# Kernel tuning notes

Hardware: AMD Instinct MI355X
Metric: run time of the kernel (lower is better)

## Reference

```python
import jax, jax.numpy as jnp
import numpy as np

N_NODES = 10000
N_EDGES = 160000
N_GRAPHS = 64
D_IN = 128
D_H = 512
N_CLS = 2
L = 3
EPS = 1e-7   # GENConv message eps / clamp min
MAXV = 10.0  # GENConv power-mean clamp max
BN_EPS = 1e-5


def setup_inputs() -> dict:
    key = jax.random.key(0)
    ks = jax.random.split(key, 8)
    return {
        "x": jax.random.normal(ks[0], (N_NODES, D_IN), jnp.float32),
        "W0": jax.random.normal(ks[1], (D_IN, D_H), jnp.float32) * 0.05,
        "Wrest": jax.random.normal(ks[2], (L - 1, D_H, D_H), jnp.float32) * 0.05,
        "bconv": jnp.zeros((L, D_H), jnp.float32),
        "p": jnp.ones((L,), jnp.float32),
        "msg_scale": jnp.ones((L,), jnp.float32),
        "bn_gamma": jnp.ones((L, D_H), jnp.float32),
        "bn_beta": jnp.zeros((L, D_H), jnp.float32),
        "fc1_W": jax.random.normal(ks[3], (2 * D_H, D_H), jnp.float32) * 0.05,
        "fc1_b": jnp.zeros((D_H,), jnp.float32),
        "bn4_g": jnp.ones((D_H,), jnp.float32),
        "bn4_b": jnp.zeros((D_H,), jnp.float32),
        "fc2_W": jax.random.normal(ks[4], (D_H, N_CLS), jnp.float32) * 0.05,
        "fc2_b": jnp.zeros((N_CLS,), jnp.float32),
        "edge_index": jax.random.randint(ks[5], (2, N_EDGES), 0, N_NODES, dtype=jnp.int32),
        "batch": jnp.sort(jax.random.randint(ks[6], (N_NODES,), 0, N_GRAPHS, dtype=jnp.int32)),
    }


def _batchnorm(h, g, b):
    # training-mode BatchNorm1d: batch statistics, biased variance
    mu = h.mean(axis=0)
    var = ((h - mu) ** 2).mean(axis=0)
    return (h - mu) * jax.lax.rsqrt(var + BN_EPS) * g + b


def _genconv(x, W, b, p, scale, src, dst):
    # message: m_e = relu(x_src) + eps  (no edge_attr), clamped to [eps, 10]
    m = jnp.minimum(jax.nn.relu(x[src]) + EPS, MAXV)          # [E, d]
    # power-mean aggregation onto target nodes
    deg = jax.ops.segment_sum(jnp.ones((src.shape[0],), x.dtype), dst, N_NODES)
    agg = jax.ops.segment_sum(m ** p, dst, N_NODES) / jnp.maximum(deg, 1.0)[:, None]
    agg = jnp.clip(agg, EPS, MAXV) ** (1.0 / p)               # [N, d]
    # MessageNorm: l2-normalize aggregated message, rescale by ||x|| * scale
    msg = agg / jnp.maximum(jnp.linalg.norm(agg, axis=-1, keepdims=True), 1e-12)
    xn = jnp.linalg.norm(x, axis=-1, keepdims=True)
    out = x + msg * xn * scale                                # residual add
    return out @ W + b                                        # 1-layer MLP


def reference(x, W0, Wrest, bconv, p, msg_scale, bn_gamma, bn_beta,
              fc1_W, fc1_b, bn4_g, bn4_b, fc2_W, fc2_b, edge_index, batch):
    src, dst = edge_index[0], edge_index[1]
    h = x
    jk = None
    for i in range(L):
        W = W0 if i == 0 else Wrest[i - 1]
        h = _genconv(h, W, bconv[i], p[i], msg_scale[i], src, dst)
        h = jax.nn.relu(_batchnorm(h, bn_gamma[i], bn_beta[i]))
        jk = h if jk is None else jnp.maximum(jk, h)          # JumpingKnowledge 'max'
    # global max + mean pooling per graph
    cnt = jax.ops.segment_sum(jnp.ones((N_NODES,), h.dtype), batch, N_GRAPHS)
    gmean = jax.ops.segment_sum(jk, batch, N_GRAPHS) / jnp.maximum(cnt, 1.0)[:, None]
    gmax = jax.ops.segment_max(jk, batch, N_GRAPHS)
    gmax = jnp.where(cnt[:, None] > 0, gmax, 0.0)
    g = jnp.concatenate([gmax, gmean], axis=1)                # [G, 1024]
    g = jax.nn.relu(_batchnorm(g @ fc1_W + fc1_b, bn4_g, bn4_b))
    # dropout: eval mode (identity)
    return g @ fc2_W + fc2_b                                  # [G, num_classes]
```

## Files before the change

### kernel.cpp

```cpp
#include <hip/hip_runtime.h>
#include <hip/hip_bf16.h>
#include <math.h>

#define N_NODES 10000
#define N_GRAPHS 64
#define N_EDGES 160000
#define D_INPUT 128
#define D_H 512
#define EPS 1e-7f
#define MAXV 10.0f
#define BN_EPS 1e-5f
#define M_PAD 10112

typedef __attribute__((ext_vector_type(4))) float f32x4;
typedef __attribute__((ext_vector_type(8))) __bf16 bf16x8;

__global__ __launch_bounds__(256) void hist_kernel(const int* __restrict__ dst,
                                                   int* __restrict__ cnt) {
  int i = blockIdx.x * blockDim.x + threadIdx.x;
  if (i < N_EDGES) atomicAdd(&cnt[dst[i]], 1);
}

__global__ __launch_bounds__(256) void scan_kernel(int* __restrict__ cnt,
                                                   int* __restrict__ rowptr) {
  __shared__ int ps[256];
  int tid = threadIdx.x;
  const int CH = 40;
  int b0 = tid * CH;
  bool active = (b0 < N_NODES);
  int v[CH];
  int s = 0;
  if (active) {
    const int4* c4p = (const int4*)(cnt + b0);
#pragma unroll
    for (int i = 0; i < CH / 4; i++) {
      int4 q = c4p[i];
      v[4 * i] = q.x; v[4 * i + 1] = q.y; v[4 * i + 2] = q.z; v[4 * i + 3] = q.w;
      s += q.x + q.y + q.z + q.w;
    }
  }
  ps[tid] = s;
  __syncthreads();
  for (int off = 1; off < 256; off <<= 1) {
    int t = (tid >= off) ? ps[tid - off] : 0;
    __syncthreads();
    ps[tid] += t;
    __syncthreads();
  }
  int run = (tid == 0) ? 0 : ps[tid - 1];
  if (active) {
    int r[CH];
#pragma unroll
    for (int i = 0; i < CH; i++) { r[i] = run; run += v[i]; }
    int4* rp = (int4*)(rowptr + b0);
    int4* cz = (int4*)(cnt + b0);
#pragma unroll
    for (int i = 0; i < CH / 4; i++) {
      rp[i] = make_int4(r[4 * i], r[4 * i + 1], r[4 * i + 2], r[4 * i + 3]);
      cz[i] = make_int4(0, 0, 0, 0);
    }
  }
  if (tid == 255) rowptr[N_NODES] = ps[255];
}

__global__ __launch_bounds__(256) void scatter_kernel(
    const int* __restrict__ src, const int* __restrict__ dst,
    const int* __restrict__ rowptr, int* __restrict__ cursor,
    int* __restrict__ csr_src) {
  int i = blockIdx.x * blockDim.x + threadIdx.x;
  if (i < N_EDGES) {
    int t = dst[i];
    int pos = rowptr[t] + atomicAdd(&cursor[t], 1);
    csr_src[pos] = src[i];
  }
}

__global__ __launch_bounds__(512) void bn_affine(float* __restrict__ stats,
                                                 const float* __restrict__ gamma,
                                                 const float* __restrict__ beta,
                                                 float* __restrict__ aff) {
  int c = threadIdx.x;
  const float invN = 1.0f / (float)N_NODES;
  float mean = stats[c] * invN;
  float var = stats[D_H + c] * invN - mean * mean;
  float sc = rsqrtf(var + BN_EPS) * gamma[c];
  aff[c] = sc;
  aff[D_H + c] = beta[c] - mean * sc;
  stats[c] = 0.f;
  stats[D_H + c] = 0.f;
}

__global__ __launch_bounds__(256) void msg0_kernel(const float* __restrict__ x,
                                                   const float* __restrict__ p_ptr,
                                                   __hip_bfloat16* __restrict__ msgb) {
  float p = *p_ptr;
  bool p1 = (p == 1.0f);
  const int total = N_NODES * D_INPUT / 2;
  for (int i = blockIdx.x * 256 + threadIdx.x; i < total; i += gridDim.x * 256) {
    float2 v = ((const float2*)x)[i];
    float m0 = fminf(fmaxf(v.x, 0.f) + EPS, MAXV);
    float m1 = fminf(fmaxf(v.y, 0.f) + EPS, MAXV);
    if (!p1) { m0 = powf(m0, p); m1 = powf(m1, p); }
    __hip_bfloat162 o;
    o.x = __float2bfloat16(m0);
    o.y = __float2bfloat16(m1);
    ((__hip_bfloat162*)msgb)[i] = o;
  }
}

template <int D, bool BN>
__global__ __launch_bounds__(256) void agg_msgnorm_kernel(
    const float* __restrict__ h, const float* __restrict__ aff,
    const __hip_bfloat16* __restrict__ msgb,
    const int* __restrict__ rowptr, const int* __restrict__ csr_src,
    const float* __restrict__ p_ptr, const float* __restrict__ scale_ptr,
    __hip_bfloat16* __restrict__ out) {
  constexpr int C = D / 2;
  constexpr int SL = 256 / C;
  int n = blockIdx.x;
  int tid = threadIdx.x;
  int col = tid % C;
  int slice = tid / C;
  int lo = rowptr[n], hi = rowptr[n + 1];
  float p = *p_ptr;
  float scale = *scale_ptr;
  bool p1 = (p == 1.0f);
  float invp = 1.0f / p;
  float inv_dg = 1.0f / fmaxf((float)(hi - lo), 1.0f);
  const float2* h2 = (const float2*)h;
  const uint* mg = (const uint*)msgb;

  __shared__ int s_src[256];
  float accx = 0.f, accy = 0.f;
  for (int base = lo; base < hi; base += 256) {
    int m = min(256, hi - base);
    __syncthreads();
    if (tid < m) s_src[tid] = csr_src[base + tid];
    __syncthreads();
    int j = slice;
    for (; j + 3 * SL < m; j += 4 * SL) {
      uint u0 = mg[(size_t)s_src[j] * C + col];
      uint u1 = mg[(size_t)s_src[j + SL] * C + col];
      uint u2 = mg[(size_t)s_src[j + 2 * SL] * C + col];
      uint u3 = mg[(size_t)s_src[j + 3 * SL] * C + col];
      accx += (__uint_as_float(u0 << 16) + __uint_as_float(u1 << 16)) +
              (__uint_as_float(u2 << 16) + __uint_as_float(u3 << 16));
      accy += (__uint_as_float(u0 & 0xFFFF0000u) + __uint_as_float(u1 & 0xFFFF0000u)) +
              (__uint_as_float(u2 & 0xFFFF0000u) + __uint_as_float(u3 & 0xFFFF0000u));
    }
    for (; j < m; j += SL) {
      uint u = mg[(size_t)s_src[j] * C + col];
      accx += __uint_as_float(u << 16);
      accy += __uint_as_float(u & 0xFFFF0000u);
    }
  }

  if constexpr (SL > 1) {
    __shared__ float sacc[2][256];
    sacc[0][tid] = accx;
    sacc[1][tid] = accy;
    __syncthreads();
    if (tid < C) {
#pragma unroll
      for (int s = 1; s < SL; s++) {
        accx += sacc[0][s * C + tid];
        accy += sacc[1][s * C + tid];
      }
    }
  }

  float a0 = 0.f, a1 = 0.f, hv0 = 0.f, hv1 = 0.f, sa = 0.f, sh = 0.f;
  if (tid < C) {
    a0 = fminf(fmaxf(accx * inv_dg, EPS), MAXV);
    a1 = fminf(fmaxf(accy * inv_dg, EPS), MAXV);
    if (!p1) { a0 = powf(a0, invp); a1 = powf(a1, invp); }
    float2 hx = h2[(size_t)n * C + tid];
    if constexpr (BN) {
      float2 s2 = ((const float2*)aff)[tid];
      float2 b2 = ((const float2*)(aff + D_H))[tid];
      hx.x = fmaxf(hx.x * s2.x + b2.x, 0.f);
      hx.y = fmaxf(hx.y * s2.y + b2.y, 0.f);
    }
    hv0 = hx.x;
    hv1 = hx.y;
    sa = a0 * a0 + a1 * a1;
    sh = hv0 * hv0 + hv1 * hv1;
  }
  for (int off = 32; off; off >>= 1) {
    sa += __shfl_down(sa, off);
    sh += __shfl_down(sh, off);
  }
  __shared__ float red[2][4];
  __shared__ float tot[2];
  int wid = tid >> 6;
  if ((tid & 63) == 0) { red[0][wid] = sa; red[1][wid] = sh; }
  __syncthreads();
  if (tid == 0) {
    tot[0] = red[0][0] + red[0][1] + red[0][2] + red[0][3];
    tot[1] = red[1][0] + red[1][1] + red[1][2] + red[1][3];
  }
  __syncthreads();
  float k = sqrtf(tot[1]) * scale / fmaxf(sqrtf(tot[0]), 1e-12f);
  if (tid < C) {
    __hip_bfloat162 o2;
    o2.x = __float2bfloat16(hv0 + a0 * k);
    o2.y = __float2bfloat16(hv1 + a1 * k);
    ((__hip_bfloat162*)out)[(size_t)n * C + tid] = o2;
  }
}

__global__ __launch_bounds__(256) void convert_all(
    const float* __restrict__ W0, const float* __restrict__ Wrest,
    __hip_bfloat16* __restrict__ w0t, __hip_bfloat16* __restrict__ w1t,
    __hip_bfloat16* __restrict__ w2t, int* __restrict__ cnt,
    float* __restrict__ stats) {
  int z = blockIdx.z;
  const float* W;
  __hip_bfloat16* Wt;
  int K;
  if (z == 0) { W = W0; Wt = w0t; K = D_INPUT; }
  else if (z == 1) { W = Wrest; Wt = w1t; K = D_H; }
  else { W = Wrest + (size_t)D_H * D_H; Wt = w2t; K = D_H; }

  if (z == 0 && blockIdx.x >= 4) {
    int bid = (blockIdx.x - 4) * 16 + blockIdx.y;
    int idx = bid * 256 + threadIdx.x;
    if (idx < N_NODES) cnt[idx] = 0;
    int sidx = idx - N_NODES;
    if (sidx >= 0 && sidx < 1024) stats[sidx] = 0.f;
    return;
  }

  __shared__ float tile[32][33];
  int k0 = blockIdx.x * 32, n0 = blockIdx.y * 32;
  int tx = threadIdx.x & 31, ty = threadIdx.x >> 5;
  for (int i = ty; i < 32; i += 8)
    tile[i][tx] = W[(size_t)(k0 + i) * D_H + n0 + tx];
  __syncthreads();
  for (int i = ty; i < 32; i += 8)
    Wt[(size_t)(n0 + i) * K + k0 + tx] = __float2bfloat16(tile[tx][i]);
}

__global__ __launch_bounds__(256) void mfma_gemm(
    const __hip_bfloat16* __restrict__ A, const __hip_bfloat16* __restrict__ Bt,
    const float* __restrict__ bias, float* __restrict__ C, float* __restrict__ stats,
    int M, int K) {
  __shared__ ushort As[128 * 64];
  __shared__ ushort Bs[128 * 64];
  __shared__ float sred[128][2];
  int tid = threadIdx.x;
  int l = tid & 63;
  int w = tid >> 6;
  int wm = w >> 1, wn = w & 1;
  int row0 = blockIdx.x * 128;
  int col0 = blockIdx.y * 128;

  f32x4 acc[4][4];
#pragma unroll
  for (int m = 0; m < 4; m++)
#pragma unroll
    for (int n = 0; n < 4; n++) acc[m][n] = (f32x4){0.f, 0.f, 0.f, 0.f};

  const ushort* Ag = (const ushort*)A;
  const ushort* Bg = (const ushort*)Bt;
  char* AsB = (char*)As;
  char* BsB = (char*)Bs;

  if (tid < 128) { sred[tid][0] = 0.f; sred[tid][1] = 0.f; }

  int srow = tid >> 3;
  int scb = (tid & 7) * 16;
  int wbyte = scb ^ ((srow & 7) << 4);
  int scol = scb >> 1;

  int lswz = (l & 7) << 4;
  int kb = (l >> 4) * 16;
  int arow = wm * 64 + (l & 15);
  int brow = wn * 64 + (l & 15);

  for (int k0 = 0; k0 < K; k0 += 64) {
    uint4 ra[4], rb[4];
#pragma unroll
    for (int j = 0; j < 4; j++) {
      int row = j * 32 + srow;
      ra[j] = *(const uint4*)(Ag + (size_t)(row0 + row) * K + k0 + scol);
      rb[j] = *(const uint4*)(Bg + (size_t)(col0 + row) * K + k0 + scol);
    }
#pragma unroll
    for (int j = 0; j < 4; j++) {
      int row = j * 32 + srow;
      *(uint4*)(AsB + row * 128 + wbyte) = ra[j];
      *(uint4*)(BsB + row * 128 + wbyte) = rb[j];
    }
    __syncthreads();
#pragma unroll
    for (int kk = 0; kk < 2; kk++) {
      bf16x8 af[4], bfr[4];
#pragma unroll
      for (int m = 0; m < 4; m++)
        af[m] = *(const bf16x8*)(AsB + (arow + m * 16) * 128 + ((kk * 64 + kb) ^ lswz));
#pragma unroll
      for (int n = 0; n < 4; n++)
        bfr[n] = *(const bf16x8*)(BsB + (brow + n * 16) * 128 + ((kk * 64 + kb) ^ lswz));
#pragma unroll
      for (int m = 0; m < 4; m++)
#pragma unroll
        for (int n = 0; n < 4; n++)
          acc[m][n] = __builtin_amdgcn_mfma_f32_16x16x32_bf16(af[m], bfr[n], acc[m][n], 0, 0, 0);
    }
    __syncthreads();
  }

  int crow0 = row0 + wm * 64 + (l >> 4) * 4;
  int ccol0 = col0 + wn * 64 + (l & 15);
#pragma unroll
  for (int n = 0; n < 4; n++) {
    int col = ccol0 + n * 16;
    float bv = bias[col];
    float ps = 0.f, pq = 0.f;
#pragma unroll
    for (int m = 0; m < 4; m++) {
#pragma unroll
      for (int r = 0; r < 4; r++) {
        int rr = crow0 + m * 16 + r;
        if (rr < M) {
          float v = acc[m][n][r] + bv;
          C[(size_t)rr * D_H + col] = v;
          ps += v;
          pq += v * v;
        }
      }
    }
    ps += __shfl_down(ps, 16); pq += __shfl_down(pq, 16);
    ps += __shfl_down(ps, 32); pq += __shfl_down(pq, 32);
    if ((l >> 4) == 0) {
      atomicAdd(&sred[wn * 64 + n * 16 + (l & 15)][0], ps);
      atomicAdd(&sred[wn * 64 + n * 16 + (l & 15)][1], pq);
    }
  }
  __syncthreads();
  if (tid < 128) {
    atomicAdd(&stats[col0 + tid], sred[tid][0]);
    atomicAdd(&stats[D_H + col0 + tid], sred[tid][1]);
  }
}

template <bool WRITE_MSG>
__global__ __launch_bounds__(256) void jk_msg_update(
    const float* __restrict__ hlin, const float* __restrict__ aff,
    float* __restrict__ jk, const float* __restrict__ p_ptr,
    __hip_bfloat16* __restrict__ msgb, int layer) {
  float p = 1.f;
  bool p1 = true;
  if constexpr (WRITE_MSG) {
    p = *p_ptr;
    p1 = (p == 1.0f);
  }
  const int total = N_NODES * D_H / 4;
  for (int idx = blockIdx.x * blockDim.x + threadIdx.x; idx < total;
       idx += gridDim.x * blockDim.x) {
    int c4 = idx & 127;
    float4 x = ((const float4*)hlin)[idx];
    float4 sc = ((const float4*)aff)[c4];
    float4 sh = ((const float4*)(aff + D_H))[c4];
    float4 v;
    v.x = fmaxf(x.x * sc.x + sh.x, 0.f);
    v.y = fmaxf(x.y * sc.y + sh.y, 0.f);
    v.z = fmaxf(x.z * sc.z + sh.z, 0.f);
    v.w = fmaxf(x.w * sc.w + sh.w, 0.f);
    if constexpr (WRITE_MSG) {
      float m0 = fminf(v.x + EPS, MAXV);
      float m1 = fminf(v.y + EPS, MAXV);
      float m2 = fminf(v.z + EPS, MAXV);
      float m3 = fminf(v.w + EPS, MAXV);
      if (!p1) { m0 = powf(m0, p); m1 = powf(m1, p); m2 = powf(m2, p); m3 = powf(m3, p); }
      __hip_bfloat162 o01, o23;
      o01.x = __float2bfloat16(m0); o01.y = __float2bfloat16(m1);
      o23.x = __float2bfloat16(m2); o23.y = __float2bfloat16(m3);
      ((__hip_bfloat162*)msgb)[2 * idx] = o01;
      ((__hip_bfloat162*)msgb)[2 * idx + 1] = o23;
    }
    if (layer != 0) {
      float4 j = ((const float4*)jk)[idx];
      v.x = fmaxf(v.x, j.x);
      v.y = fmaxf(v.y, j.y);
      v.z = fmaxf(v.z, j.z);
      v.w = fmaxf(v.w, j.w);
    }
    ((float4*)jk)[idx] = v;
  }
}

__device__ __forceinline__ int lower_bound_i(const int* a, int n, int v) {
  int lo = 0, hi = n;
  while (lo < hi) {
    int mid = (lo + hi) >> 1;
    if (a[mid] < v) lo = mid + 1; else hi = mid;
  }
  return lo;
}

__global__ __launch_bounds__(256) void pool_kernel(const float* __restrict__ jk,
                                                   const int* __restrict__ batch,
                                                   float* __restrict__ g) {
  int gid = blockIdx.x;
  int cl = threadIdx.x & 15;
  int slice = threadIdx.x >> 4;
  int f4c = blockIdx.y * 16 + cl;
  int lo = lower_bound_i(batch, N_NODES, gid);
  int hi = lower_bound_i(batch, N_NODES, gid + 1);
  const float4* J = (const float4*)jk;
  float4 mx = make_float4(0.f, 0.f, 0.f, 0.f);
  float4 sm = make_float4(0.f, 0.f, 0.f, 0.f);
  int r = lo + slice;
  for (; r + 16 < hi; r += 32) {
    float4 v0 = J[(size_t)r * 128 + f4c];
    float4 v1 = J[(size_t)(r + 16) * 128 + f4c];
    mx.x = fmaxf(fmaxf(mx.x, v0.x), v1.x);
    mx.y = fmaxf(fmaxf(mx.y, v0.y), v1.y);
    mx.z = fmaxf(fmaxf(mx.z, v0.z), v1.z);
    mx.w = fmaxf(fmaxf(mx.w, v0.w), v1.w);
    sm.x += v0.x + v1.x; sm.y += v0.y + v1.y;
    sm.z += v0.z + v1.z; sm.w += v0.w + v1.w;
  }
  for (; r < hi; r += 16) {
    float4 v = J[(size_t)r * 128 + f4c];
    mx.x = fmaxf(mx.x, v.x); mx.y = fmaxf(mx.y, v.y);
    mx.z = fmaxf(mx.z, v.z); mx.w = fmaxf(mx.w, v.w);
    sm.x += v.x; sm.y += v.y; sm.z += v.z; sm.w += v.w;
  }
  __shared__ float4 smax[16][16];
  __shared__ float4 ssum[16][16];
  smax[slice][cl] = mx;
  ssum[slice][cl] = sm;
  __syncthreads();
  if (slice == 0) {
#pragma unroll
    for (int s = 1; s < 16; s++) {
      float4 m2 = smax[s][cl], s2 = ssum[s][cl];
      mx.x = fmaxf(mx.x, m2.x); mx.y = fmaxf(mx.y, m2.y);
      mx.z = fmaxf(mx.z, m2.z); mx.w = fmaxf(mx.w, m2.w);
      sm.x += s2.x; sm.y += s2.y; sm.z += s2.z; sm.w += s2.w;
    }
    float ic = 1.0f / fmaxf((float)(hi - lo), 1.0f);
    if (hi <= lo) mx = make_float4(0.f, 0.f, 0.f, 0.f);
    sm.x *= ic; sm.y *= ic; sm.z *= ic; sm.w *= ic;
    ((float4*)(g + (size_t)gid * 1024))[f4c] = mx;
    ((float4*)(g + (size_t)gid * 1024 + D_H))[f4c] = sm;
  }
}

__global__ __launch_bounds__(256) void fc1_kernel(const float* __restrict__ g,
                                                  const float* __restrict__ W,
                                                  const float* __restrict__ b,
                                                  float* __restrict__ out) {
  __shared__ float sg[1024];
  __shared__ float sred[4][64];
  int gid = blockIdx.x;
  int tid = threadIdx.x;
  ((float4*)sg)[tid] = ((const float4*)(g + (size_t)gid * 1024))[tid];
  __syncthreads();
  int cl = tid & 63;
  int slice = tid >> 6;
  int col = blockIdx.y * 64 + cl;
  int k0 = slice * 256;
  float acc = 0.f;
#pragma unroll 4
  for (int k = k0; k < k0 + 256; k++) acc += sg[k] * W[(size_t)k * D_H + col];
  sred[slice][cl] = acc;
  __syncthreads();
  if (slice == 0)
    out[(size_t)gid * D_H + col] =
        sred[0][cl] + sred[1][cl] + sred[2][cl] + sred[3][cl] + b[col];
}

__global__ __launch_bounds__(256) void bn4_kernel(const float* __restrict__ x,
                                                  const float* __restrict__ gmm,
                                                  const float* __restrict__ bb,
                                                  float* __restrict__ y) {
  int cl = threadIdx.x & 63;
  int slice = threadIdx.x >> 6;
  int c = blockIdx.x * 64 + cl;
  float s = 0.f, q = 0.f;
#pragma unroll
  for (int r = slice * 16; r < slice * 16 + 16; r++) {
    float v = x[(size_t)r * D_H + c];
    s += v; q += v * v;
  }
  __shared__ float ss[4][64], sq[4][64];
  ss[slice][cl] = s;
  sq[slice][cl] = q;
  __syncthreads();
  float S = ss[0][cl] + ss[1][cl] + ss[2][cl] + ss[3][cl];
  float Q = sq[0][cl] + sq[1][cl] + sq[2][cl] + sq[3][cl];
  float mean = S * (1.0f / N_GRAPHS);
  float var = Q * (1.0f / N_GRAPHS) - mean * mean;
  float rs = rsqrtf(var + BN_EPS) * gmm[c];
  float sh = bb[c] - mean * rs;
#pragma unroll
  for (int r = slice * 16; r < slice * 16 + 16; r++)
    y[(size_t)r * D_H + c] = fmaxf(x[(size_t)r * D_H + c] * rs + sh, 0.f);
}

__global__ __launch_bounds__(64) void fc2_kernel(const float* __restrict__ y,
                                                 const float* __restrict__ W,
                                                 const float* __restrict__ b,
                                                 float* __restrict__ out) {
  int gid = blockIdx.x;
  int lane = threadIdx.x;
  float a0 = 0.f, a1 = 0.f;
  for (int k = lane; k < D_H; k += 64) {
    float v = y[(size_t)gid * D_H + k];
    a0 += v * W[k * 2 + 0];
    a1 += v * W[k * 2 + 1];
  }
  for (int off = 32; off; off >>= 1) {
    a0 += __shfl_down(a0, off);
    a1 += __shfl_down(a1, off);
  }
  if (lane == 0) {
    out[gid * 2 + 0] = a0 + b[0];
    out[gid * 2 + 1] = a1 + b[1];
  }
}

extern "C" void kernel_launch(void* const* d_in, const int* in_sizes, int n_in,
                              void* d_out, int out_size, void* d_ws, size_t ws_size,
                              hipStream_t stream) {
  const float* x       = (const float*)d_in[0];
  const float* W0      = (const float*)d_in[1];
  const float* Wrest   = (const float*)d_in[2];
  const float* bconv   = (const float*)d_in[3];
  const float* p       = (const float*)d_in[4];
  const float* mscale  = (const float*)d_in[5];
  const float* bn_g    = (const float*)d_in[6];
  const float* bn_b    = (const float*)d_in[7];
  const float* fc1_W   = (const float*)d_in[8];
  const float* fc1_b   = (const float*)d_in[9];
  const float* bn4_g   = (const float*)d_in[10];
  const float* bn4_b   = (const float*)d_in[11];
  const float* fc2_W   = (const float*)d_in[12];
  const float* fc2_b   = (const float*)d_in[13];
  const int*   eidx    = (const int*)d_in[14];
  const int*   batch   = (const int*)d_in[15];
  float* out = (float*)d_out;

  const int* src = eidx;
  const int* dst = eidx + N_EDGES;

  float* ws = (float*)d_ws;
  const size_t NH = (size_t)N_NODES * D_H;
  float* hlin  = ws;
  float* jk    = hlin + NH;
  float* stats = jk + NH;
  float* aff   = stats + 1024;
  __hip_bfloat16* residb = (__hip_bfloat16*)(aff + 1024);
  __hip_bfloat16* msgb = residb + (size_t)M_PAD * D_H;
  __hip_bfloat16* w0t = msgb + NH;
  __hip_bfloat16* w1t = w0t + 512 * 128;
  __hip_bfloat16* w2t = w1t + 512 * 512;
  int* cnt     = (int*)(w2t + 512 * 512);
  int* rowptr  = cnt + N_NODES;
  int* csr_src = rowptr + N_NODES + 1;
  float* g     = (float*)(csr_src + N_EDGES);
  float* g2lin = g + 64 * 1024;
  float* g2    = g2lin + 64 * D_H;

  convert_all<<<dim3(16, 16, 3), 256, 0, stream>>>(W0, Wrest, w0t, w1t, w2t, cnt, stats);

  hist_kernel<<<(N_EDGES + 255) / 256, 256, 0, stream>>>(dst, cnt);
  scan_kernel<<<1, 256, 0, stream>>>(cnt, rowptr);
  scatter_kernel<<<(N_EDGES + 255) / 256, 256, 0, stream>>>(src, dst, rowptr, cnt, csr_src);

  msg0_kernel<<<1280, 256, 0, stream>>>(x, p, msgb);

  for (int layer = 0; layer < 3; layer++) {
    if (layer == 0)
      agg_msgnorm_kernel<D_INPUT, false><<<N_NODES, 256, 0, stream>>>(
          x, nullptr, msgb, rowptr, csr_src, p + layer, mscale + layer, residb);
    else
      agg_msgnorm_kernel<D_H, true><<<N_NODES, 256, 0, stream>>>(
          hlin, aff, msgb, rowptr, csr_src, p + layer, mscale + layer, residb);
    const __hip_bfloat16* Wt = (layer == 0) ? w0t : (layer == 1 ? w1t : w2t);
    int K = (layer == 0) ? D_INPUT : D_H;
    mfma_gemm<<<dim3(M_PAD / 128, D_H / 128), 256, 0, stream>>>(
        residb, Wt, bconv + (size_t)layer * D_H, hlin, stats, N_NODES, K);
    bn_affine<<<1, 512, 0, stream>>>(stats, bn_g + (size_t)layer * D_H,
                                     bn_b + (size_t)layer * D_H, aff);
    if (layer < 2)
      jk_msg_update<true><<<2048, 256, 0, stream>>>(hlin, aff, jk, p + layer + 1, msgb, layer);
    else
      jk_msg_update<false><<<2048, 256, 0, stream>>>(hlin, aff, jk, nullptr, nullptr, layer);
  }

  pool_kernel<<<dim3(N_GRAPHS, 8), 256, 0, stream>>>(jk, batch, g);
  fc1_kernel<<<dim3(N_GRAPHS, 8), 256, 0, stream>>>(g, fc1_W, fc1_b, g2lin);
  bn4_kernel<<<8, 256, 0, stream>>>(g2lin, bn4_g, bn4_b, g2);
  fc2_kernel<<<N_GRAPHS, 64, 0, stream>>>(g2, fc2_W, fc2_b, out);
}
```

Baseline: 255.9 us.

## Fuse BatchNorm, JK-max and message prep into GEMM via grid barrier

The GEMM kernel now keeps its accumulators in registers, waits at a software grid-wide barrier (an atomic counter with spin) until all 316 blocks have added their column statistics, then applies BN, ReLU and JK max and writes the next layer's bf16 messages directly. This removes the fp32 hlin round trip and the separate bn_affine and jk_msg_update launches. The histogram and msg0 kernels are merged, BN4 is folded into fc1 (stats via atomics) and fc2, and the aggregation indices are premultiplied. The barrier only works if all blocks are co-resident, which launch_bounds(256,2) is meant to allow; if they are not, the kernel deadlocks.

```diff
diff --git a/kernel.cpp b/kernel.cpp
--- a/kernel.cpp
+++ b/kernel.cpp
@@ -11,14 +11,35 @@
 #define MAXV 10.0f
 #define BN_EPS 1e-5f
 #define M_PAD 10112
+#define GEMM_BLOCKS 316
 
 typedef __attribute__((ext_vector_type(4))) float f32x4;
 typedef __attribute__((ext_vector_type(8))) __bf16 bf16x8;
 
-__global__ __launch_bounds__(256) void hist_kernel(const int* __restrict__ dst,
-                                                   int* __restrict__ cnt) {
-  int i = blockIdx.x * blockDim.x + threadIdx.x;
-  if (i < N_EDGES) atomicAdd(&cnt[dst[i]], 1);
+__global__ __launch_bounds__(256) void hist_msg0(const int* __restrict__ dst,
+                                                 int* __restrict__ cnt,
+                                                 const float* __restrict__ x,
+                                                 const float* __restrict__ p_ptr,
+                                                 __hip_bfloat16* __restrict__ msgb) {
+  int bid = blockIdx.x;
+  int tid = threadIdx.x;
+  if (bid < 625) {
+    atomicAdd(&cnt[dst[bid * 256 + tid]], 1);
+    return;
+  }
+  float p = *p_ptr;
+  bool p1 = (p == 1.0f);
+  const int total = N_NODES * D_INPUT / 2;
+  for (int i = (bid - 625) * 256 + tid; i < total; i += 320000) {
+    float2 v = ((const float2*)x)[i];
+    float m0 = fminf(fmaxf(v.x, 0.f) + EPS, MAXV);
+    float m1 = fminf(fmaxf(v.y, 0.f) + EPS, MAXV);
+    if (!p1) { m0 = powf(m0, p); m1 = powf(m1, p); }
+    __hip_bfloat162 o;
+    o.x = __float2bfloat16(m0);
+    o.y = __float2bfloat16(m1);
+    ((__hip_bfloat162*)msgb)[i] = o;
+  }
 }
 
 __global__ __launch_bounds__(256) void scan_kernel(int* __restrict__ cnt,
@@ -75,43 +96,9 @@
   }
 }
 
-__global__ __launch_bounds__(512) void bn_affine(float* __restrict__ stats,
-                                                 const float* __restrict__ gamma,
-                                                 const float* __restrict__ beta,
-                                                 float* __restrict__ aff) {
-  int c = threadIdx.x;
-  const float invN = 1.0f / (float)N_NODES;
-  float mean = stats[c] * invN;
-  float var = stats[D_H + c] * invN - mean * mean;
-  float sc = rsqrtf(var + BN_EPS) * gamma[c];
-  aff[c] = sc;
-  aff[D_H + c] = beta[c] - mean * sc;
-  stats[c] = 0.f;
-  stats[D_H + c] = 0.f;
-}
-
-__global__ __launch_bounds__(256) void msg0_kernel(const float* __restrict__ x,
-                                                   const float* __restrict__ p_ptr,
-                                                   __hip_bfloat16* __restrict__ msgb) {
-  float p = *p_ptr;
-  bool p1 = (p == 1.0f);
-  const int total = N_NODES * D_INPUT / 2;
-  for (int i = blockIdx.x * 256 + threadIdx.x; i < total; i += gridDim.x * 256) {
-    float2 v = ((const float2*)x)[i];
-    float m0 = fminf(fmaxf(v.x, 0.f) + EPS, MAXV);
-    float m1 = fminf(fmaxf(v.y, 0.f) + EPS, MAXV);
-    if (!p1) { m0 = powf(m0, p); m1 = powf(m1, p); }
-    __hip_bfloat162 o;
-    o.x = __float2bfloat16(m0);
-    o.y = __float2bfloat16(m1);
-    ((__hip_bfloat162*)msgb)[i] = o;
-  }
-}
-
-template <int D, bool BN>
+template <int D>
 __global__ __launch_bounds__(256) void agg_msgnorm_kernel(
-    const float* __restrict__ h, const float* __restrict__ aff,
-    const __hip_bfloat16* __restrict__ msgb,
+    const float* __restrict__ h, const __hip_bfloat16* __restrict__ msgb,
     const int* __restrict__ rowptr, const int* __restrict__ csr_src,
     const float* __restrict__ p_ptr, const float* __restrict__ scale_ptr,
     __hip_bfloat16* __restrict__ out) {
@@ -135,21 +122,21 @@
   for (int base = lo; base < hi; base += 256) {
     int m = min(256, hi - base);
     __syncthreads();
-    if (tid < m) s_src[tid] = csr_src[base + tid];
+    if (tid < m) s_src[tid] = csr_src[base + tid] * C;
     __syncthreads();
     int j = slice;
     for (; j + 3 * SL < m; j += 4 * SL) {
-      uint u0 = mg[(size_t)s_src[j] * C + col];
-      uint u1 = mg[(size_t)s_src[j + SL] * C + col];
-      uint u2 = mg[(size_t)s_src[j + 2 * SL] * C + col];
-      uint u3 = mg[(size_t)s_src[j + 3 * SL] * C + col];
+      uint u0 = mg[s_src[j] + col];
+      uint u1 = mg[s_src[j + SL] + col];
+      uint u2 = mg[s_src[j + 2 * SL] + col];
+      uint u3 = mg[s_src[j + 3 * SL] + col];
       accx += (__uint_as_float(u0 << 16) + __uint_as_float(u1 << 16)) +
               (__uint_as_float(u2 << 16) + __uint_as_float(u3 << 16));
       accy += (__uint_as_float(u0 & 0xFFFF0000u) + __uint_as_float(u1 & 0xFFFF0000u)) +
               (__uint_as_float(u2 & 0xFFFF0000u) + __uint_as_float(u3 & 0xFFFF0000u));
     }
     for (; j < m; j += SL) {
-      uint u = mg[(size_t)s_src[j] * C + col];
+      uint u = mg[s_src[j] + col];
       accx += __uint_as_float(u << 16);
       accy += __uint_as_float(u & 0xFFFF0000u);
     }
@@ -175,12 +162,6 @@
     a1 = fminf(fmaxf(accy * inv_dg, EPS), MAXV);
     if (!p1) { a0 = powf(a0, invp); a1 = powf(a1, invp); }
     float2 hx = h2[(size_t)n * C + tid];
-    if constexpr (BN) {
-      float2 s2 = ((const float2*)aff)[tid];
-      float2 b2 = ((const float2*)(aff + D_H))[tid];
-      hx.x = fmaxf(hx.x * s2.x + b2.x, 0.f);
-      hx.y = fmaxf(hx.y * s2.y + b2.y, 0.f);
-    }
     hv0 = hx.x;
     hv1 = hx.y;
     sa = a0 * a0 + a1 * a1;
@@ -213,7 +194,8 @@
     const float* __restrict__ W0, const float* __restrict__ Wrest,
     __hip_bfloat16* __restrict__ w0t, __hip_bfloat16* __restrict__ w1t,
     __hip_bfloat16* __restrict__ w2t, int* __restrict__ cnt,
-    float* __restrict__ stats) {
+    float* __restrict__ stats, float* __restrict__ stats4,
+    int* __restrict__ done) {
   int z = blockIdx.z;
   const float* W;
   __hip_bfloat16* Wt;
@@ -223,11 +205,14 @@
   else { W = Wrest + (size_t)D_H * D_H; Wt = w2t; K = D_H; }
 
   if (z == 0 && blockIdx.x >= 4) {
-    int bid = (blockIdx.x - 4) * 16 + blockIdx.y;
-    int idx = bid * 256 + threadIdx.x;
-    if (idx < N_NODES) cnt[idx] = 0;
-    int sidx = idx - N_NODES;
-    if (sidx >= 0 && sidx < 1024) stats[sidx] = 0.f;
+    int e = ((blockIdx.x - 4) * 16 + blockIdx.y) * 256 + threadIdx.x;
+    if (e < 10000) cnt[e] = 0;
+    else {
+      int f = e - 10000;
+      if (f < 3072) stats[f] = 0.f;
+      else if (f < 4096) stats4[f - 3072] = 0.f;
+      else if (f < 4100) done[f - 4096] = 0;
+    }
     return;
   }
 
@@ -241,10 +226,14 @@
     Wt[(size_t)(n0 + i) * K + k0 + tx] = __float2bfloat16(tile[tx][i]);
 }
 
-__global__ __launch_bounds__(256) void mfma_gemm(
+template <int LAYER>
+__global__ __launch_bounds__(256, 2) void mfma_gemm_fused(
     const __hip_bfloat16* __restrict__ A, const __hip_bfloat16* __restrict__ Bt,
-    const float* __restrict__ bias, float* __restrict__ C, float* __restrict__ stats,
-    int M, int K) {
+    const float* __restrict__ bias, float* __restrict__ stats,
+    const float* __restrict__ gamma, const float* __restrict__ beta,
+    float* __restrict__ hout, const float* __restrict__ jk_in,
+    float* __restrict__ jk_out, const float* __restrict__ p_ptr,
+    __hip_bfloat16* __restrict__ msgb, int* __restrict__ done, int M, int K) {
   __shared__ ushort As[128 * 64];
   __shared__ ushort Bs[128 * 64];
   __shared__ float sred[128][2];
@@ -313,6 +302,7 @@
 
   int crow0 = row0 + wm * 64 + (l >> 4) * 4;
   int ccol0 = col0 + wn * 64 + (l & 15);
+
 #pragma unroll
   for (int n = 0; n < 4; n++) {
     int col = ccol0 + n * 16;
@@ -325,7 +315,6 @@
         int rr = crow0 + m * 16 + r;
         if (rr < M) {
           float v = acc[m][n][r] + bv;
-          C[(size_t)rr * D_H + col] = v;
           ps += v;
           pq += v * v;
         }
@@ -343,51 +332,62 @@
     atomicAdd(&stats[col0 + tid], sred[tid][0]);
     atomicAdd(&stats[D_H + col0 + tid], sred[tid][1]);
   }
-}
-
-template <bool WRITE_MSG>
-__global__ __launch_bounds__(256) void jk_msg_update(
-    const float* __restrict__ hlin, const float* __restrict__ aff,
-    float* __restrict__ jk, const float* __restrict__ p_ptr,
-    __hip_bfloat16* __restrict__ msgb, int layer) {
-  float p = 1.f;
+
+  __threadfence();
+  __syncthreads();
+  if (tid == 0) {
+    atomicAdd(done, 1);
+    while (atomicAdd(done, 0) < GEMM_BLOCKS) __builtin_amdgcn_s_sleep(8);
+  }
+  __syncthreads();
+
+  float* sstat = (float*)As;
+  {
+    int c = tid & 127;
+    int which = tid >> 7;
+    sstat[tid] = atomicAdd(&stats[which * D_H + col0 + c], 0.0f);
+  }
+  __syncthreads();
+
+  const float invN = 1.0f / (float)N_NODES;
+  float pnext = 1.f;
   bool p1 = true;
-  if constexpr (WRITE_MSG) {
-    p = *p_ptr;
-    p1 = (p == 1.0f);
-  }
-  const int total = N_NODES * D_H / 4;
-  for (int idx = blockIdx.x * blockDim.x + threadIdx.x; idx < total;
-       idx += gridDim.x * blockDim.x) {
-    int c4 = idx & 127;
-    float4 x = ((const float4*)hlin)[idx];
-    float4 sc = ((const float4*)aff)[c4];
-    float4 sh = ((const float4*)(aff + D_H))[c4];
-    float4 v;
-    v.x = fmaxf(x.x * sc.x + sh.x, 0.f);
-    v.y = fmaxf(x.y * sc.y + sh.y, 0.f);
-    v.z = fmaxf(x.z * sc.z + sh.z, 0.f);
-    v.w = fmaxf(x.w * sc.w + sh.w, 0.f);
-    if constexpr (WRITE_MSG) {
-      float m0 = fminf(v.x + EPS, MAXV);
-      float m1 = fminf(v.y + EPS, MAXV);
-      float m2 = fminf(v.z + EPS, MAXV);
-      float m3 = fminf(v.w + EPS, MAXV);
-      if (!p1) { m0 = powf(m0, p); m1 = powf(m1, p); m2 = powf(m2, p); m3 = powf(m3, p); }
-      __hip_bfloat162 o01, o23;
-      o01.x = __float2bfloat16(m0); o01.y = __float2bfloat16(m1);
-      o23.x = __float2bfloat16(m2); o23.y = __float2bfloat16(m3);
-      ((__hip_bfloat162*)msgb)[2 * idx] = o01;
-      ((__hip_bfloat162*)msgb)[2 * idx + 1] = o23;
-    }
-    if (layer != 0) {
-      float4 j = ((const float4*)jk)[idx];
-      v.x = fmaxf(v.x, j.x);
-      v.y = fmaxf(v.y, j.y);
-      v.z = fmaxf(v.z, j.z);
-      v.w = fmaxf(v.w, j.w);
-    }
-    ((float4*)jk)[idx] = v;
+  if constexpr (LAYER < 2) {
+    pnext = *p_ptr;
+    p1 = (pnext == 1.0f);
+  }
+#pragma unroll
+  for (int n = 0; n < 4; n++) {
+    int col = ccol0 + n * 16;
+    float bv = bias[col];
+    float mean = sstat[col - col0] * invN;
+    float var = sstat[128 + col - col0] * invN - mean * mean;
+    float sc = rsqrtf(var + BN_EPS) * gamma[col];
+    float shf = beta[col] - mean * sc;
+#pragma unroll
+    for (int m = 0; m < 4; m++) {
+#pragma unroll
+      for (int r = 0; r < 4; r++) {
+        int rr = crow0 + m * 16 + r;
+        if (rr < M) {
+          size_t idx = (size_t)rr * D_H + col;
+          float v = fmaxf((acc[m][n][r] + bv) * sc + shf, 0.f);
+          if constexpr (LAYER == 0) {
+            hout[idx] = v;
+          } else if constexpr (LAYER == 1) {
+            hout[idx] = v;
+            jk_out[idx] = fmaxf(jk_in[idx], v);
+          } else {
+            hout[idx] = fmaxf(jk_in[idx], v);
+          }
+          if constexpr (LAYER < 2) {
+            float mm = fminf(v + EPS, MAXV);
+            if (!p1) mm = powf(mm, pnext);
+            msgb[idx] = __float2bfloat16(mm);
+          }
+        }
+      }
+    }
   }
 }
 
@@ -453,7 +453,8 @@
 __global__ __launch_bounds__(256) void fc1_kernel(const float* __restrict__ g,
                                                   const float* __restrict__ W,
                                                   const float* __restrict__ b,
-                                                  float* __restrict__ out) {
+                                                  float* __restrict__ out,
+                                                  float* __restrict__ stats4) {
   __shared__ float sg[1024];
   __shared__ float sred[4][64];
   int gid = blockIdx.x;
@@ -469,48 +470,32 @@
   for (int k = k0; k < k0 + 256; k++) acc += sg[k] * W[(size_t)k * D_H + col];
   sred[slice][cl] = acc;
   __syncthreads();
-  if (slice == 0)
-    out[(size_t)gid * D_H + col] =
-        sred[0][cl] + sred[1][cl] + sred[2][cl] + sred[3][cl] + b[col];
-}
-
-__global__ __launch_bounds__(256) void bn4_kernel(const float* __restrict__ x,
-                                                  const float* __restrict__ gmm,
-                                                  const float* __restrict__ bb,
-                                                  float* __restrict__ y) {
-  int cl = threadIdx.x & 63;
-  int slice = threadIdx.x >> 6;
-  int c = blockIdx.x * 64 + cl;
-  float s = 0.f, q = 0.f;
-#pragma unroll
-  for (int r = slice * 16; r < slice * 16 + 16; r++) {
-    float v = x[(size_t)r * D_H + c];
-    s += v; q += v * v;
-  }
-  __shared__ float ss[4][64], sq[4][64];
-  ss[slice][cl] = s;
-  sq[slice][cl] = q;
-  __syncthreads();
-  float S = ss[0][cl] + ss[1][cl] + ss[2][cl] + ss[3][cl];
-  float Q = sq[0][cl] + sq[1][cl] + sq[2][cl] + sq[3][cl];
-  float mean = S * (1.0f / N_GRAPHS);
-  float var = Q * (1.0f / N_GRAPHS) - mean * mean;
-  float rs = rsqrtf(var + BN_EPS) * gmm[c];
-  float sh = bb[c] - mean * rs;
-#pragma unroll
-  for (int r = slice * 16; r < slice * 16 + 16; r++)
-    y[(size_t)r * D_H + c] = fmaxf(x[(size_t)r * D_H + c] * rs + sh, 0.f);
+  if (slice == 0) {
+    float v = sred[0][cl] + sred[1][cl] + sred[2][cl] + sred[3][cl] + b[col];
+    out[(size_t)gid * D_H + col] = v;
+    atomicAdd(&stats4[col], v);
+    atomicAdd(&stats4[D_H + col], v * v);
+  }
 }
 
 __global__ __launch_bounds__(64) void fc2_kernel(const float* __restrict__ y,
+                                                 const float* __restrict__ stats4,
+                                                 const float* __restrict__ gmm,
+                                                 const float* __restrict__ bb,
                                                  const float* __restrict__ W,
                                                  const float* __restrict__ b,
                                                  float* __restrict__ out) {
   int gid = blockIdx.x;
   int lane = threadIdx.x;
+  const float invG = 1.0f / (float)N_GRAPHS;
   float a0 = 0.f, a1 = 0.f;
-  for (int k = lane; k < D_H; k += 64) {
-    float v = y[(size_t)gid * D_H + k];
+#pragma unroll
+  for (int j = 0; j < 8; j++) {
+    int k = lane + j * 64;
+    float mean = stats4[k] * invG;
+    float var = stats4[D_H + k] * invG - mean * mean;
+    float sc = rsqrtf(var + BN_EPS) * gmm[k];
+    float v = fmaxf(y[(size_t)gid * D_H + k] * sc + bb[k] - mean * sc, 0.f);
     a0 += v * W[k * 2 + 0];
     a1 += v * W[k * 2 + 1];
   }
@@ -550,11 +535,13 @@
 
   float* ws = (float*)d_ws;
   const size_t NH = (size_t)N_NODES * D_H;
-  float* hlin  = ws;
-  float* jk    = hlin + NH;
-  float* stats = jk + NH;
-  float* aff   = stats + 1024;
-  __hip_bfloat16* residb = (__hip_bfloat16*)(aff + 1024);
+  float* h0     = ws;
+  float* h1     = h0 + NH;
+  float* jk     = h1 + NH;
+  float* stats  = jk + NH;
+  float* stats4 = stats + 3072;
+  int*   done   = (int*)(stats4 + 1024);
+  __hip_bfloat16* residb = (__hip_bfloat16*)(done + 4);
   __hip_bfloat16* msgb = residb + (size_t)M_PAD * D_H;
   __hip_bfloat16* w0t = msgb + NH;
   __hip_bfloat16* w1t = w0t + 512 * 128;
@@ -564,37 +551,32 @@
   int* csr_src = rowptr + N_NODES + 1;
   float* g     = (float*)(csr_src + N_EDGES);
   float* g2lin = g + 64 * 1024;
-  float* g2    = g2lin + 64 * D_H;
-
-  convert_all<<<dim3(16, 16, 3), 256, 0, stream>>>(W0, Wrest, w0t, w1t, w2t, cnt, stats);
-
-  hist_kernel<<<(N_EDGES + 255) / 256, 256, 0, stream>>>(dst, cnt);
+
+  convert_all<<<dim3(16, 16, 3), 256, 0, stream>>>(W0, Wrest, w0t, w1t, w2t,
+                                                   cnt, stats, stats4, done);
+  hist_msg0<<<1875, 256, 0, stream>>>(dst, cnt, x, p, msgb);
   scan_kernel<<<1, 256, 0, stream>>>(cnt, rowptr);
   scatter_kernel<<<(N_EDGES + 255) / 256, 256, 0, stream>>>(src, dst, rowptr, cnt, csr_src);
 
-  msg0_kernel<<<1280, 256, 0, stream>>>(x, p, msgb);
-
-  for (int layer = 0; layer < 3; layer++) {
-    if (layer == 0)
-      agg_msgnorm_kernel<D_INPUT, false><<<N_NODES, 256, 0, stream>>>(
-          x, nullptr, msgb, rowptr, csr_src, p + layer, mscale + layer, residb);
-    else
-      agg_msgnorm_kernel<D_H, true><<<N_NODES, 256, 0, stream>>>(
-          hlin, aff, msgb, rowptr, csr_src, p + layer, mscale + layer, residb);
-    const __hip_bfloat16* Wt = (layer == 0) ? w0t : (layer == 1 ? w1t : w2t);
-    int K = (layer == 0) ? D_INPUT : D_H;
-    mfma_gemm<<<dim3(M_PAD / 128, D_H / 128), 256, 0, stream>>>(
-        residb, Wt, bconv + (size_t)layer * D_H, hlin, stats, N_NODES, K);
-    bn_affine<<<1, 512, 0, stream>>>(stats, bn_g + (size_t)layer * D_H,
-                                     bn_b + (size_t)layer * D_H, aff);
-    if (layer < 2)
-      jk_msg_update<true><<<2048, 256, 0, stream>>>(hlin, aff, jk, p + layer + 1, msgb, layer);
-    else
-      jk_msg_update<false><<<2048, 256, 0, stream>>>(hlin, aff, jk, nullptr, nullptr, layer);
-  }
-
-  pool_kernel<<<dim3(N_GRAPHS, 8), 256, 0, stream>>>(jk, batch, g);
-  fc1_kernel<<<dim3(N_GRAPHS, 8), 256, 0, stream>>>(g, fc1_W, fc1_b, g2lin);
-  bn4_kernel<<<8, 256, 0, stream>>>(g2lin, bn4_g, bn4_b, g2);
-  fc2_kernel<<<N_GRAPHS, 64, 0, stream>>>(g2, fc2_W, fc2_b, out);
-}
+  agg_msgnorm_kernel<D_INPUT><<<N_NODES, 256, 0, stream>>>(
+      x, msgb, rowptr, csr_src, p + 0, mscale + 0, residb);
+  mfma_gemm_fused<0><<<dim3(79, 4), 256, 0, stream>>>(
+      residb, w0t, bconv, stats, bn_g, bn_b,
+      h0, nullptr, nullptr, p + 1, msgb, done + 0, N_NODES, D_INPUT);
+
+  agg_msgnorm_kernel<D_H><<<N_NODES, 256, 0, stream>>>(
+      h0, msgb, rowptr, csr_src, p + 1, mscale + 1, residb);
+  mfma_gemm_fused<1><<<dim3(79, 4), 256, 0, stream>>>(
+      residb, w1t, bconv + D_H, stats + 1024, bn_g + D_H, bn_b + D_H,
+      h1, h0, jk, p + 2, msgb, done + 1, N_NODES, D_H);
+
+  agg_msgnorm_kernel<D_H><<<N_NODES, 256, 0, stream>>>(
+      h1, msgb, rowptr, csr_src, p + 2, mscale + 2, residb);
+  mfma_gemm_fused<2><<<dim3(79, 4), 256, 0, stream>>>(
+      residb, w2t, bconv + 2 * D_H, stats + 2048, bn_g + 2 * D_H, bn_b + 2 * D_H,
+      h0 , jk, nullptr, nullptr, nullptr, done + 2, N_NODES, D_H);
+
+  pool_kernel<<<dim3(N_GRAPHS, 8), 256, 0, stream>>>(h0, batch, g);
+  fc1_kernel<<<dim3(N_GRAPHS, 8), 256, 0, stream>>>(g, fc1_W, fc1_b, g2lin, stats4);
+  fc2_kernel<<<N_GRAPHS, 64, 0, stream>>>(g2lin, stats4, bn4_g, bn4_b, fc2_W, fc2_b, out);
+}
```

Result: slower. 362.9 us (+41.8%).
